# Performance work log

Measured on AMD Instinct MI355X. Metric: run time of the kernel, lower is better.

Reference implementation:

```python
import jax, jax.numpy as jnp
import numpy as np

N = 50000; E = 800000; NFEAT = 128; NHID = 64; CONCAT = 2; NCLASS = 40
D = CONCAT * NHID
BN_EPS = 1e-5


def setup_inputs() -> dict:
    key = jax.random.key(0)
    ks = jax.random.split(key, 16)
    rn = lambda k, s, sc=0.05: jax.random.normal(k, s, jnp.float32) * sc
    return {
        "x1a": rn(ks[0], (N, NFEAT), 1.0),
        "x1b": rn(ks[1], (N, NFEAT), 1.0),
        "x2a": rn(ks[2], (N, NFEAT), 1.0),
        "x2b": rn(ks[3], (N, NFEAT), 1.0),
        "edge_index1": jax.random.randint(ks[4], (2, E), 0, N),
        "edge_index2": jax.random.randint(ks[5], (2, E), 0, N),
        "Wi": rn(ks[6], (CONCAT, NFEAT, NHID)),
        "bi": jnp.zeros((CONCAT, NHID), jnp.float32),
        "gi": jnp.ones((CONCAT, NHID), jnp.float32),
        "bei": jnp.zeros((CONCAT, NHID), jnp.float32),
        "Wm": rn(ks[7], (2, D, D)),
        "bm": jnp.zeros((2, D), jnp.float32),
        "gm": jnp.ones((2, D), jnp.float32),
        "bem": jnp.zeros((2, D), jnp.float32),
        "Wf": rn(ks[8], (D, NCLASS)),
        "bf": jnp.zeros((NCLASS,), jnp.float32),
        "fc1w1_W": rn(ks[9], (D,)),
        "fc1w1_b": jnp.zeros((1,), jnp.float32),
        "fc1w2_W": rn(ks[10], (D,)),
        "fc1w2_b": jnp.zeros((1,), jnp.float32),
        "aws_w1_W": rn(ks[11], (2, D)),
        "aws_w1_b": jnp.zeros((2,), jnp.float32),
        "aws_w2_W": rn(ks[12], (2, D)),
        "aws_w2_b": jnp.zeros((2,), jnp.float32),
        "fcw1_W": rn(ks[13], (NCLASS,)),
        "fcw1_b": jnp.zeros((1,), jnp.float32),
        "fcw2_W": rn(ks[14], (NCLASS,)),
        "fcw2_b": jnp.zeros((1,), jnp.float32),
    }


def _gcn_norm(edge_index, n):
    # GCN symmetric normalization with self-loops (cached=True behaviour)
    loop = jnp.arange(n)
    src = jnp.concatenate([edge_index[0], loop])
    dst = jnp.concatenate([edge_index[1], loop])
    deg = jax.ops.segment_sum(jnp.ones_like(dst, jnp.float32), dst, n)
    dinv = jnp.where(deg > 0, deg ** -0.5, 0.0)
    return src, dst, dinv[src] * dinv[dst]


def _gcn(x, W, b, g):
    # GCNConv: dense projection then sparse scatter-based aggregation
    src, dst, norm = g
    h = x @ W
    agg = jax.ops.segment_sum(h[src] * norm[:, None], dst, x.shape[0])
    return agg + b


def _bn(x, gamma, beta):
    m = x.mean(0)
    v = jnp.mean((x - m) ** 2, axis=0)
    return (x - m) * jax.lax.rsqrt(v + BN_EPS) * gamma + beta


def _gate(x1, x2, w1, b1, w2, b2):
    # sigmoid gates L1-normalized; only the last node's row is used (w[-1,:])
    s1 = jax.nn.sigmoid(jnp.dot(x1[-1], w1) + b1)
    s2 = jax.nn.sigmoid(jnp.dot(x2[-1], w2) + b2)
    t = s1 + s2
    return s1 / t, s2 / t


def _forward(x1a, x1b, x2a, x2b, g1, g2, Wi, bi, gi, bei, Wm, bm, gm, bem,
             Wf, bf, fc1w1_W, fc1w1_b, fc1w2_W, fc1w2_b,
             aws_w1_W, aws_w1_b, aws_w2_W, aws_w2_b,
             fcw1_W, fcw1_b, fcw2_W, fcw2_b):
    xs1, xs2 = (x1a, x1b), (x2a, x2b)
    h1 = jnp.concatenate([jax.nn.relu(_bn(_gcn(xs1[i], Wi[i], bi[i], g1), gi[i], bei[i]))
                          for i in range(CONCAT)], axis=-1)
    h2 = jnp.concatenate([jax.nn.relu(_bn(_gcn(xs2[i], Wi[i], bi[i], g2), gi[i], bei[i]))
                          for i in range(CONCAT)], axis=-1)
    w1, w2 = _gate(h1, h2, fc1w1_W, fc1w1_b[0], fc1w2_W, fc1w2_b[0])
    x = w1 * h1 + w2 * h2
    for i in range(Wm.shape[0]):  # middle layers (n_layers - 2)
        a = jax.nn.relu(_bn(_gcn(x, Wm[i], bm[i], g1), gm[i], bem[i]))
        b = jax.nn.relu(_bn(_gcn(x, Wm[i], bm[i], g2), gm[i], bem[i]))
        w1, w2 = _gate(a, b, aws_w1_W[i], aws_w1_b[i], aws_w2_W[i], aws_w2_b[i])
        x = w1 * a + w2 * b
    p1 = _gcn(x, Wf, bf, g1)
    p2 = _gcn(x, Wf, bf, g2)
    w1, w2 = _gate(p1, p2, fcw1_W, fcw1_b[0], fcw2_W, fcw2_b[0])
    return (w1 * p1 + w2 * p2, p1, p2)


def reference(x1a, x1b, x2a, x2b, edge_index1, edge_index2, Wi, bi, gi, bei,
              Wm, bm, gm, bem, Wf, bf, fc1w1_W, fc1w1_b, fc1w2_W, fc1w2_b,
              aws_w1_W, aws_w1_b, aws_w2_W, aws_w2_b,
              fcw1_W, fcw1_b, fcw2_W, fcw2_b):
    g1 = _gcn_norm(edge_index1, N)
    g2 = _gcn_norm(edge_index2, N)
    return _forward(x1a, x1b, x2a, x2b, g1, g2, Wi, bi, gi, bei, Wm, bm, gm, bem,
                    Wf, bf, fc1w1_W, fc1w1_b, fc1w2_W, fc1w2_b,
                    aws_w1_W, aws_w1_b, aws_w2_W, aws_w2_b,
                    fcw1_W, fcw1_b, fcw2_W, fcw2_b)
```

## Files before the change

kernel.cpp:

```cpp
#include <hip/hip_runtime.h>
#include <hip/hip_fp16.h>


#define DFEAT 128

typedef __attribute__((ext_vector_type(8))) short bf16x8;
typedef __attribute__((ext_vector_type(4))) float f32x4;

__device__ __forceinline__ unsigned short f2bf(float f) {
    unsigned u = __float_as_uint(f);
    u += 0x7fffu + ((u >> 16) & 1u);
    return (unsigned short)(u >> 16);
}
__device__ __forceinline__ float bf2f(unsigned short u) {
    return __uint_as_float((unsigned)u << 16);
}
__device__ __forceinline__ float4 bf4tof4(ushort4 u) {
    return make_float4(__uint_as_float((unsigned)u.x << 16),
                       __uint_as_float((unsigned)u.y << 16),
                       __uint_as_float((unsigned)u.z << 16),
                       __uint_as_float((unsigned)u.w << 16));
}
__device__ __forceinline__ unsigned f2h16(float f) {
    return (unsigned)__half_as_ushort(__float2half(f));
}
__device__ __forceinline__ float h16f(unsigned u) {
    return __half2float(__ushort_as_half((unsigned short)u));
}

constexpr int RANGES = 8;
constexpr int SLICES = 32;
constexpr int MAXRSZ = 6400;

__global__ __launch_bounds__(256) void histRS_kernel(
    const int* __restrict__ dst1, const int* __restrict__ dst2,
    int* __restrict__ base, int n, int E, int rsz) {
    int range = blockIdx.x & (RANGES - 1);
    int q = blockIdx.x >> 3;
    int slice = q & (SLICES - 1);
    int graph = q >> 5;
    const int* dst = graph ? dst2 : dst1;
    int r0 = range * rsz;
    int rn = min(rsz, n - r0);
    if (rn <= 0) return;
    __shared__ int hist[MAXRSZ];
    int t = threadIdx.x;
    for (int i = t; i < rn; i += 256) hist[i] = 0;
    __syncthreads();
    int es = (E + SLICES - 1) / SLICES;
    int e0 = slice * es;
    int e1 = min(e0 + es, E);
    for (int i = e0 + t; i < e1; i += 256) {
        unsigned d = (unsigned)(dst[i] - r0);
        if (d < (unsigned)rn) atomicAdd(&hist[d], 1);
    }
    __syncthreads();
    int* bp = base + (size_t)(graph * SLICES + slice) * n + r0;
    for (int i = t; i < rn; i += 256) bp[i] = hist[i];
}

__global__ __launch_bounds__(256) void slicescan_kernel(
    int* __restrict__ base, int* __restrict__ cnt1, int* __restrict__ cnt2, int n) {
    int node = blockIdx.x * 256 + threadIdx.x;
    int g = blockIdx.y;
    if (node >= n) return;
    int* p = base + (size_t)g * SLICES * n + node;
    int run = 0;
#pragma unroll
    for (int s = 0; s < SLICES; ++s) {
        int v = p[(size_t)s * n];
        p[(size_t)s * n] = run;
        run += v;
    }
    (g ? cnt2 : cnt1)[node] = run;
}

__global__ __launch_bounds__(256) void fillRS_kernel(
    const int* __restrict__ src1, const int* __restrict__ dst1,
    const int* __restrict__ src2, const int* __restrict__ dst2,
    const int* __restrict__ base,
    const int* __restrict__ rp1, const int* __restrict__ rp2,
    const float* __restrict__ dv1, const float* __restrict__ dv2,
    int* __restrict__ cs1, int* __restrict__ cs2, int n, int E, int rsz) {
    int range = blockIdx.x & (RANGES - 1);
    int q = blockIdx.x >> 3;
    int slice = q & (SLICES - 1);
    int graph = q >> 5;
    const int *src, *dst, *rp;
    const float* dv;
    int* cs;
    if (graph == 0) { src = src1; dst = dst1; rp = rp1; dv = dv1; cs = cs1; }
    else            { src = src2; dst = dst2; rp = rp2; dv = dv2; cs = cs2; }
    int r0 = range * rsz;
    int rn = min(rsz, n - r0);
    if (rn <= 0) return;
    __shared__ int off[MAXRSZ];
    int t = threadIdx.x;
    const int* bp = base + (size_t)(graph * SLICES + slice) * n + r0;
    for (int i = t; i < rn; i += 256) off[i] = bp[i] + rp[r0 + i];
    __syncthreads();
    int es = (E + SLICES - 1) / SLICES;
    int e0 = slice * es;
    int e1 = min(e0 + es, E);
    for (int i = e0 + t; i < e1; i += 256) {
        int d = dst[i];
        unsigned dr = (unsigned)(d - r0);
        if (dr < (unsigned)rn) {
            int s = src[i];
            float w = dv[d] * dv[s];
            int pos = atomicAdd(&off[dr], 1);
            cs[pos] = (int)((f2h16(w) << 16) | (unsigned)s);
        }
    }
}

__global__ __launch_bounds__(256) void blocksum_kernel(const int* __restrict__ c1,
                                                       const int* __restrict__ c2,
                                                       int* __restrict__ bs, int n, int nb) {
    const int* c = blockIdx.y ? c2 : c1;
    int* out = bs + (size_t)blockIdx.y * nb;
    int t = threadIdx.x;
    int base = blockIdx.x * 2048 + t * 8;
    int s = 0;
#pragma unroll
    for (int i = 0; i < 8; ++i) {
        int idx = base + i;
        if (idx < n) s += c[idx];
    }
    __shared__ int red[256];
    red[t] = s;
    __syncthreads();
    for (int o = 128; o > 0; o >>= 1) {
        if (t < o) red[t] += red[t + o];
        __syncthreads();
    }
    if (t == 0) out[blockIdx.x] = red[0];
}

__global__ void scansums_kernel(int* __restrict__ bs, int nb, int* __restrict__ rp1,
                                int* __restrict__ rp2, int n, int E, float* __restrict__ stats) {
    int t = threadIdx.x;
    if (t < 2) {
        int* b = bs + (size_t)t * nb;
        int run = 0;
        for (int i = 0; i < nb; ++i) {
            int v = b[i];
            b[i] = run;
            run += v;
        }
        (t ? rp2 : rp1)[n] = E;
    }
    for (int i = t; i < 512; i += 64) stats[i] = 0.f;
}

__global__ __launch_bounds__(256) void writerp_kernel(const int* __restrict__ c1,
                                                      const int* __restrict__ c2,
                                                      const int* __restrict__ bs,
                                                      int* __restrict__ rp1, int* __restrict__ rp2,
                                                      float* __restrict__ dv1,
                                                      float* __restrict__ dv2, int n, int nb) {
    const int* c = blockIdx.y ? c2 : c1;
    int* rp = blockIdx.y ? rp2 : rp1;
    float* dv = blockIdx.y ? dv2 : dv1;
    int boff = bs[(size_t)blockIdx.y * nb + blockIdx.x];
    int t = threadIdx.x;
    int base = blockIdx.x * 2048 + t * 8;
    int v[8];
    int s = 0;
#pragma unroll
    for (int i = 0; i < 8; ++i) {
        int idx = base + i;
        v[i] = (idx < n) ? c[idx] : 0;
        s += v[i];
    }
    __shared__ int red[256];
    red[t] = s;
    __syncthreads();
    for (int o = 1; o < 256; o <<= 1) {
        int x = (t >= o) ? red[t - o] : 0;
        __syncthreads();
        red[t] += x;
        __syncthreads();
    }
    int run = boff + red[t] - s;
#pragma unroll
    for (int i = 0; i < 8; ++i) {
        int idx = base + i;
        if (idx < n) {
            rp[idx] = run;
            dv[idx] = rsqrtf((float)(v[i] + 1));
            run += v[i];
        }
    }
}

template <int FV, typename OutT>
__global__ __launch_bounds__(256) void dualagg_kernel(
    const unsigned short* __restrict__ h1, const unsigned short* __restrict__ h2,
    const int* __restrict__ rp1, const int* __restrict__ cs1, const float* __restrict__ dv1,
    const int* __restrict__ rp2, const int* __restrict__ cs2, const float* __restrict__ dv2,
    const float* __restrict__ bias, OutT* __restrict__ o1, OutT* __restrict__ o2, int n) {
    constexpr int COLS = FV * 4;
    const unsigned short* h;
    const int *rp, *cs;
    const float* dv;
    OutT* out;
    if (blockIdx.y == 0) { h = h1; rp = rp1; cs = cs1; dv = dv1; out = o1; }
    else                 { h = h2; rp = rp2; cs = cs2; dv = dv2; out = o2; }
    int wid = blockIdx.x * 4 + (threadIdx.x >> 6);
    if (wid >= n) return;
    int lane = threadIdx.x & 63;
    int half = lane >> 5;
    int l = lane & 31;
    bool act = (l < FV);
    float4 acc = make_float4(0.f, 0.f, 0.f, 0.f);
    int e0 = rp[wid], e1 = rp[wid + 1];
    int e = e0 + half;
    for (; e + 6 < e1; e += 8) {
        int va = cs[e], vb = cs[e + 2], vc = cs[e + 4], vd = cs[e + 6];
        float wa = h16f((unsigned)va >> 16); int sa = va & 0xFFFF;
        float wb = h16f((unsigned)vb >> 16); int sb = vb & 0xFFFF;
        float wc = h16f((unsigned)vc >> 16); int sc = vc & 0xFFFF;
        float wd = h16f((unsigned)vd >> 16); int sd = vd & 0xFFFF;
        if (act) {
            float4 ha = bf4tof4(((const ushort4*)(h + (size_t)sa * COLS))[l]);
            float4 hb = bf4tof4(((const ushort4*)(h + (size_t)sb * COLS))[l]);
            float4 hc = bf4tof4(((const ushort4*)(h + (size_t)sc * COLS))[l]);
            float4 hd = bf4tof4(((const ushort4*)(h + (size_t)sd * COLS))[l]);
            acc.x = fmaf(wa, ha.x, acc.x); acc.y = fmaf(wa, ha.y, acc.y);
            acc.z = fmaf(wa, ha.z, acc.z); acc.w = fmaf(wa, ha.w, acc.w);
            acc.x = fmaf(wb, hb.x, acc.x); acc.y = fmaf(wb, hb.y, acc.y);
            acc.z = fmaf(wb, hb.z, acc.z); acc.w = fmaf(wb, hb.w, acc.w);
            acc.x = fmaf(wc, hc.x, acc.x); acc.y = fmaf(wc, hc.y, acc.y);
            acc.z = fmaf(wc, hc.z, acc.z); acc.w = fmaf(wc, hc.w, acc.w);
            acc.x = fmaf(wd, hd.x, acc.x); acc.y = fmaf(wd, hd.y, acc.y);
            acc.z = fmaf(wd, hd.z, acc.z); acc.w = fmaf(wd, hd.w, acc.w);
        }
    }
    for (; e < e1; e += 2) {
        int va = cs[e];
        float wa = h16f((unsigned)va >> 16); int sa = va & 0xFFFF;
        if (act) {
            float4 ha = bf4tof4(((const ushort4*)(h + (size_t)sa * COLS))[l]);
            acc.x = fmaf(wa, ha.x, acc.x); acc.y = fmaf(wa, ha.y, acc.y);
            acc.z = fmaf(wa, ha.z, acc.z); acc.w = fmaf(wa, ha.w, acc.w);
        }
    }
    acc.x += __shfl_xor(acc.x, 32);
    acc.y += __shfl_xor(acc.y, 32);
    acc.z += __shfl_xor(acc.z, 32);
    acc.w += __shfl_xor(acc.w, 32);
    if (half == 0 && act) {
        float dn = dv[wid];
        float w = dn * dn;
        float4 hv = bf4tof4(((const ushort4*)(h + (size_t)wid * COLS))[l]);
        acc.x = fmaf(w, hv.x, acc.x); acc.y = fmaf(w, hv.y, acc.y);
        acc.z = fmaf(w, hv.z, acc.z); acc.w = fmaf(w, hv.w, acc.w);
        float4 b = ((const float4*)bias)[l];
        acc.x += b.x; acc.y += b.y; acc.z += b.z; acc.w += b.w;
        if constexpr (sizeof(OutT) == 4) {
            ((float4*)((float*)out + (size_t)wid * COLS))[l] = acc;
        } else {
            ushort4 o;
            o.x = f2bf(acc.x); o.y = f2bf(acc.y); o.z = f2bf(acc.z); o.w = f2bf(acc.w);
            ((ushort4*)((unsigned short*)out + (size_t)wid * COLS))[l] = o;
        }
    }
}

__global__ __launch_bounds__(256) void gemm_l1_kernel(
    const float* __restrict__ x1a, const float* __restrict__ x1b, const float* __restrict__ x2a,
    const float* __restrict__ x2b, const float* __restrict__ Wi, unsigned short* __restrict__ H1,
    unsigned short* __restrict__ H2, int nrows) {
    constexpr int CG = 16;
    const float* X = (blockIdx.y == 0) ? x1a : (blockIdx.y == 1) ? x1b
                     : (blockIdx.y == 2) ? x2a : x2b;
    const float* W = Wi + (blockIdx.y & 1) * 128 * 64;
    unsigned short* Y = (blockIdx.y < 2) ? H1 : H2;
    int ocol = (int)(blockIdx.y & 1) * 64;
    __shared__ float Ws[32][64];
    __shared__ float Xs[64][32];
    int tid = threadIdx.x;
    int row0 = blockIdx.x * 64;
    int cg = tid % CG;
    int rg = tid / CG;
    float4 acc[4];
#pragma unroll
    for (int i = 0; i < 4; ++i) acc[i] = make_float4(0.f, 0.f, 0.f, 0.f);
    for (int kc = 0; kc < 4; ++kc) {
        for (int i = tid; i < 32 * CG; i += 256) {
            int r = i / CG, c = i % CG;
            *(float4*)&Ws[r][c * 4] = *(const float4*)(W + (size_t)(kc * 32 + r) * 64 + c * 4);
        }
        for (int i = tid; i < 64 * 8; i += 256) {
            int r = i / 8, c = i % 8;
            int gr = row0 + r;
            float4 v = make_float4(0.f, 0.f, 0.f, 0.f);
            if (gr < nrows) v = *(const float4*)(X + (size_t)gr * DFEAT + kc * 32 + c * 4);
            *(float4*)&Xs[r][c * 4] = v;
        }
        __syncthreads();
#pragma unroll
        for (int k = 0; k < 32; ++k) {
            float4 w = *(float4*)&Ws[k][cg * 4];
#pragma unroll
            for (int i = 0; i < 4; ++i) {
                float a = Xs[rg * 4 + i][k];
                acc[i].x = fmaf(a, w.x, acc[i].x);
                acc[i].y = fmaf(a, w.y, acc[i].y);
                acc[i].z = fmaf(a, w.z, acc[i].z);
                acc[i].w = fmaf(a, w.w, acc[i].w);
            }
        }
        __syncthreads();
    }
#pragma unroll
    for (int i = 0; i < 4; ++i) {
        int r = row0 + rg * 4 + i;
        if (r < nrows) {
            ushort4 o;
            o.x = f2bf(acc[i].x); o.y = f2bf(acc[i].y);
            o.z = f2bf(acc[i].z); o.w = f2bf(acc[i].w);
            *(ushort4*)(Y + (size_t)r * DFEAT + ocol + cg * 4) = o;
        }
    }
}

__global__ __launch_bounds__(256) void prepW_kernel(const float* __restrict__ Wm,
                                                    unsigned short* __restrict__ Wt) {
    int o = blockIdx.x * 256 + threadIdx.x;
    int l = blockIdx.y;
    int kk = o & 31;
    int col = (o >> 5) & 127;
    int kc = o >> 12;
    int k = kc * 32 + kk;
    Wt[(size_t)l * 16384 + o] = f2bf(Wm[(size_t)l * 16384 + (size_t)k * 128 + col]);
}

__global__ __launch_bounds__(256) void gemm_mfma_kernel(
    const unsigned short* __restrict__ Abf, const unsigned short* __restrict__ Bbf,
    const float* __restrict__ ss, const float* __restrict__ wout,
    const unsigned short* __restrict__ Wt, unsigned short* __restrict__ Y, int nrows) {
    __shared__ short Xs[64][128];
    int tid = threadIdx.x;
    int row0 = blockIdx.x * 64;
    int wave = tid >> 6, lane = tid & 63;
    int m = lane & 15, quad = lane >> 4;
    float w1 = wout[0], w2 = wout[1];
    for (int u = tid; u < 1024; u += 256) {
        int r = u >> 4;
        int col0 = (u & 15) * 8;
        int gr = row0 + r;
        if (gr < nrows) {
#pragma unroll
            for (int hh = 0; hh < 2; ++hh) {
                int c = col0 + hh * 4;
                float4 fa = bf4tof4(*(const ushort4*)(Abf + (size_t)gr * 128 + c));
                float4 fb = bf4tof4(*(const ushort4*)(Bbf + (size_t)gr * 128 + c));
                float4 sa = *(const float4*)(ss + c);
                float4 ha = *(const float4*)(ss + 128 + c);
                float4 sb = *(const float4*)(ss + 256 + c);
                float4 hb = *(const float4*)(ss + 384 + c);
                ushort4 o;
                o.x = f2bf(w1 * fmaxf(fmaf(fa.x, sa.x, ha.x), 0.f) +
                           w2 * fmaxf(fmaf(fb.x, sb.x, hb.x), 0.f));
                o.y = f2bf(w1 * fmaxf(fmaf(fa.y, sa.y, ha.y), 0.f) +
                           w2 * fmaxf(fmaf(fb.y, sb.y, hb.y), 0.f));
                o.z = f2bf(w1 * fmaxf(fmaf(fa.z, sa.z, ha.z), 0.f) +
                           w2 * fmaxf(fmaf(fb.z, sb.z, hb.z), 0.f));
                o.w = f2bf(w1 * fmaxf(fmaf(fa.w, sa.w, ha.w), 0.f) +
                           w2 * fmaxf(fmaf(fb.w, sb.w, hb.w), 0.f));
                *(ushort4*)&Xs[r][c] = o;
            }
        } else {
            ushort4 z = {0, 0, 0, 0};
            *(ushort4*)&Xs[r][col0] = z;
            *(ushort4*)&Xs[r][col0 + 4] = z;
        }
    }
    __syncthreads();
    f32x4 acc[8];
#pragma unroll
    for (int i = 0; i < 8; ++i) acc[i] = (f32x4){0.f, 0.f, 0.f, 0.f};
#pragma unroll
    for (int kc = 0; kc < 4; ++kc) {
        bf16x8 a = *(const bf16x8*)&Xs[wave * 16 + m][kc * 32 + quad * 8];
#pragma unroll
        for (int ct = 0; ct < 8; ++ct) {
            const short* bp = (const short*)(Wt + ((size_t)(kc * 128 + ct * 16 + m) * 32) + quad * 8);
            bf16x8 b = *(const bf16x8*)bp;
            acc[ct] = __builtin_amdgcn_mfma_f32_16x16x32_bf16(a, b, acc[ct], 0, 0, 0);
        }
    }
#pragma unroll
    for (int ct = 0; ct < 8; ++ct) {
#pragma unroll
        for (int i = 0; i < 4; ++i) {
            int gr = row0 + wave * 16 + quad * 4 + i;
            if (gr < nrows) Y[(size_t)gr * 128 + ct * 16 + m] = f2bf(acc[ct][i]);
        }
    }
}

template <int CG, int RPT>
__global__ __launch_bounds__(256) void gemm_fused_kernel(
    const unsigned short* __restrict__ Abf, const unsigned short* __restrict__ Bbf,
    const float* __restrict__ ss, const float* __restrict__ wout, const float* __restrict__ W,
    unsigned short* __restrict__ Y, int nrows, int fout, int ostride) {
    __shared__ float Ws[32][CG * 4];
    __shared__ float Xs[64][32];
    int tid = threadIdx.x;
    int row0 = blockIdx.x * 64;
    int cg = tid % CG;
    int rg = tid / CG;
    float w1 = wout[0], w2 = wout[1];
    float4 acc[RPT];
#pragma unroll
    for (int i = 0; i < RPT; ++i) acc[i] = make_float4(0.f, 0.f, 0.f, 0.f);
    for (int kc = 0; kc < 4; ++kc) {
        for (int i = tid; i < 32 * CG; i += 256) {
            int r = i / CG, c = i % CG;
            float4 w;
            if ((c * 4 + 3) < fout) {
                w = *(const float4*)(W + (size_t)(kc * 32 + r) * fout + c * 4);
            } else {
                float t0 = (c * 4 + 0) < fout ? W[(size_t)(kc * 32 + r) * fout + c * 4 + 0] : 0.f;
                float t1 = (c * 4 + 1) < fout ? W[(size_t)(kc * 32 + r) * fout + c * 4 + 1] : 0.f;
                float t2 = (c * 4 + 2) < fout ? W[(size_t)(kc * 32 + r) * fout + c * 4 + 2] : 0.f;
                float t3 = (c * 4 + 3) < fout ? W[(size_t)(kc * 32 + r) * fout + c * 4 + 3] : 0.f;
                w = make_float4(t0, t1, t2, t3);
            }
            *(float4*)&Ws[r][c * 4] = w;
        }
        for (int i = tid; i < 64 * 8; i += 256) {
            int r = i / 8, c = i % 8;
            int gr = row0 + r;
            int col0 = kc * 32 + c * 4;
            float4 v = make_float4(0.f, 0.f, 0.f, 0.f);
            if (gr < nrows) {
                float4 a = bf4tof4(*(const ushort4*)(Abf + (size_t)gr * DFEAT + col0));
                float4 b = bf4tof4(*(const ushort4*)(Bbf + (size_t)gr * DFEAT + col0));
                float4 scA = *(const float4*)(ss + col0);
                float4 shA = *(const float4*)(ss + DFEAT + col0);
                float4 scB = *(const float4*)(ss + 2 * DFEAT + col0);
                float4 shB = *(const float4*)(ss + 3 * DFEAT + col0);
                v.x = w1 * fmaxf(fmaf(a.x, scA.x, shA.x), 0.f) +
                      w2 * fmaxf(fmaf(b.x, scB.x, shB.x), 0.f);
                v.y = w1 * fmaxf(fmaf(a.y, scA.y, shA.y), 0.f) +
                      w2 * fmaxf(fmaf(b.y, scB.y, shB.y), 0.f);
                v.z = w1 * fmaxf(fmaf(a.z, scA.z, shA.z), 0.f) +
                      w2 * fmaxf(fmaf(b.z, scB.z, shB.z), 0.f);
                v.w = w1 * fmaxf(fmaf(a.w, scA.w, shA.w), 0.f) +
                      w2 * fmaxf(fmaf(b.w, scB.w, shB.w), 0.f);
            }
            *(float4*)&Xs[r][c * 4] = v;
        }
        __syncthreads();
#pragma unroll
        for (int k = 0; k < 32; ++k) {
            float4 w = *(float4*)&Ws[k][cg * 4];
#pragma unroll
            for (int i = 0; i < RPT; ++i) {
                float a = Xs[rg * RPT + i][k];
                acc[i].x = fmaf(a, w.x, acc[i].x);
                acc[i].y = fmaf(a, w.y, acc[i].y);
                acc[i].z = fmaf(a, w.z, acc[i].z);
                acc[i].w = fmaf(a, w.w, acc[i].w);
            }
        }
        __syncthreads();
    }
    if (cg * 4 < fout) {
#pragma unroll
        for (int i = 0; i < RPT; ++i) {
            int r = row0 + rg * RPT + i;
            if (r < nrows) {
                ushort4 o;
                o.x = f2bf(acc[i].x); o.y = f2bf(acc[i].y);
                o.z = f2bf(acc[i].z); o.w = f2bf(acc[i].w);
                *(ushort4*)(Y + (size_t)r * ostride + cg * 4) = o;
            }
        }
    }
}

__global__ __launch_bounds__(256) void stats2_kernel(const unsigned short* __restrict__ A,
                                                     const unsigned short* __restrict__ B,
                                                     float* __restrict__ stats, int nrows) {
    __shared__ float red1[256];
    __shared__ float red2[256];
    int t = threadIdx.x;
    int col = t & 127;
    int rg = t >> 7;
    const unsigned short* src = (blockIdx.y == 0) ? A : B;
    float* st = stats + (size_t)blockIdx.y * 256;
    int r0 = blockIdx.x * 128 + rg * 64;
    int r1 = min(r0 + 64, nrows);
    float s = 0.f, s2 = 0.f;
    for (int r = r0; r < r1; ++r) {
        float v = bf2f(src[(size_t)r * DFEAT + col]);
        s += v;
        s2 = fmaf(v, v, s2);
    }
    red1[t] = s;
    red2[t] = s2;
    __syncthreads();
    if (t < 128) {
        atomicAdd(&st[col], red1[t] + red1[t + 128]);
        atomicAdd(&st[DFEAT + col], red2[t] + red2[t + 128]);
    }
}

__global__ __launch_bounds__(128) void gate_prep_kernel(
    float* __restrict__ statsA, float* __restrict__ statsB,
    const unsigned short* __restrict__ preA, const unsigned short* __restrict__ preB,
    const float* __restrict__ gamma, const float* __restrict__ beta,
    const float* __restrict__ gwA, const float* __restrict__ gbA,
    const float* __restrict__ gwB, const float* __restrict__ gbB,
    float* __restrict__ ss, float* __restrict__ wout, int nrows) {
    __shared__ float red[128];
    __shared__ float dotA_s;
    int t = threadIdx.x;
    float invN = 1.f / (float)nrows;
    float meanA = statsA[t] * invN;
    float varA = statsA[DFEAT + t] * invN - meanA * meanA;
    float scA = gamma[t] * rsqrtf(varA + 1e-5f);
    float shA = beta[t] - meanA * scA;
    ss[t] = scA;
    ss[DFEAT + t] = shA;
    float meanB = statsB[t] * invN;
    float varB = statsB[DFEAT + t] * invN - meanB * meanB;
    float scB = gamma[t] * rsqrtf(varB + 1e-5f);
    float shB = beta[t] - meanB * scB;
    ss[2 * DFEAT + t] = scB;
    ss[3 * DFEAT + t] = shB;
    statsA[t] = 0.f;
    statsA[DFEAT + t] = 0.f;
    statsB[t] = 0.f;
    statsB[DFEAT + t] = 0.f;
    float av = fmaxf(fmaf(bf2f(preA[(size_t)(nrows - 1) * DFEAT + t]), scA, shA), 0.f);
    red[t] = av * gwA[t];
    __syncthreads();
    for (int s = 64; s > 0; s >>= 1) {
        if (t < s) red[t] += red[t + s];
        __syncthreads();
    }
    if (t == 0) dotA_s = red[0];
    __syncthreads();
    float bv = fmaxf(fmaf(bf2f(preB[(size_t)(nrows - 1) * DFEAT + t]), scB, shB), 0.f);
    red[t] = bv * gwB[t];
    __syncthreads();
    for (int s = 64; s > 0; s >>= 1) {
        if (t < s) red[t] += red[t + s];
        __syncthreads();
    }
    if (t == 0) {
        float s1 = 1.f / (1.f + expf(-(dotA_s + gbA[0])));
        float s2 = 1.f / (1.f + expf(-(red[0] + gbB[0])));
        float tt = s1 + s2;
        wout[0] = s1 / tt;
        wout[1] = s2 / tt;
    }
}

__global__ __launch_bounds__(64) void gate_final_kernel(
    const float* __restrict__ p1, const float* __restrict__ p2,
    const float* __restrict__ w1v, const float* __restrict__ b1,
    const float* __restrict__ w2v, const float* __restrict__ b2,
    float* __restrict__ wout, int nrows, int nclass) {
    __shared__ float red[64];
    __shared__ float dot1_s;
    int t = threadIdx.x;
    float v = (t < nclass) ? p1[(size_t)(nrows - 1) * nclass + t] * w1v[t] : 0.f;
    red[t] = v;
    __syncthreads();
    for (int s = 32; s > 0; s >>= 1) {
        if (t < s) red[t] += red[t + s];
        __syncthreads();
    }
    if (t == 0) dot1_s = red[0];
    __syncthreads();
    v = (t < nclass) ? p2[(size_t)(nrows - 1) * nclass + t] * w2v[t] : 0.f;
    red[t] = v;
    __syncthreads();
    for (int s = 32; s > 0; s >>= 1) {
        if (t < s) red[t] += red[t + s];
        __syncthreads();
    }
    if (t == 0) {
        float s1 = 1.f / (1.f + expf(-(dot1_s + b1[0])));
        float s2 = 1.f / (1.f + expf(-(red[0] + b2[0])));
        float tt = s1 + s2;
        wout[0] = s1 / tt;
        wout[1] = s2 / tt;
    }
}

__global__ __launch_bounds__(256) void mix_kernel(const float* __restrict__ p1,
                                                  const float* __restrict__ p2,
                                                  const float* __restrict__ wout,
                                                  float* __restrict__ o, int n4) {
    int idx = blockIdx.x * blockDim.x + threadIdx.x;
    if (idx >= n4) return;
    float w1 = wout[0], w2 = wout[1];
    float4 a = *(const float4*)(p1 + (size_t)idx * 4);
    float4 b = *(const float4*)(p2 + (size_t)idx * 4);
    float4 r = make_float4(w1 * a.x + w2 * b.x, w1 * a.y + w2 * b.y, w1 * a.z + w2 * b.z,
                           w1 * a.w + w2 * b.w);
    *(float4*)(o + (size_t)idx * 4) = r;
}

extern "C" void kernel_launch(void* const* d_in, const int* in_sizes, int n_in, void* d_out,
                              int out_size, void* d_ws, size_t ws_size, hipStream_t stream) {
    (void)n_in; (void)out_size; (void)ws_size;
    const int N = in_sizes[0] / DFEAT;
    const int E = in_sizes[4] / 2;
    const int NC = in_sizes[15];

    const float* x1a = (const float*)d_in[0];
    const float* x1b = (const float*)d_in[1];
    const float* x2a = (const float*)d_in[2];
    const float* x2b = (const float*)d_in[3];
    const int* ei1 = (const int*)d_in[4];
    const int* ei2 = (const int*)d_in[5];
    const float* Wi = (const float*)d_in[6];
    const float* bi = (const float*)d_in[7];
    const float* gi = (const float*)d_in[8];
    const float* bei = (const float*)d_in[9];
    const float* Wm = (const float*)d_in[10];
    const float* bm = (const float*)d_in[11];
    const float* gm = (const float*)d_in[12];
    const float* bem = (const float*)d_in[13];
    const float* Wf = (const float*)d_in[14];
    const float* bf = (const float*)d_in[15];
    const float* fc1w1_W = (const float*)d_in[16];
    const float* fc1w1_b = (const float*)d_in[17];
    const float* fc1w2_W = (const float*)d_in[18];
    const float* fc1w2_b = (const float*)d_in[19];
    const float* aws_w1_W = (const float*)d_in[20];
    const float* aws_w1_b = (const float*)d_in[21];
    const float* aws_w2_W = (const float*)d_in[22];
    const float* aws_w2_b = (const float*)d_in[23];
    const float* fcw1_W = (const float*)d_in[24];
    const float* fcw1_b = (const float*)d_in[25];
    const float* fcw2_W = (const float*)d_in[26];
    const float* fcw2_b = (const float*)d_in[27];

    char* ws = (char*)d_ws;
    size_t off = 0;
    auto alloc = [&](size_t bytes) -> char* {
        char* p = ws + off;
        off += (bytes + 255) & ~(size_t)255;
        return p;
    };
    unsigned short* A = (unsigned short*)alloc((size_t)N * DFEAT * 2);
    unsigned short* B = (unsigned short*)alloc((size_t)N * DFEAT * 2);
    unsigned short* H1 = (unsigned short*)alloc((size_t)N * DFEAT * 2);
    unsigned short* H2 = (unsigned short*)alloc((size_t)N * DFEAT * 2);
    int* rp1 = (int*)alloc((size_t)(N + 1) * 4);
    int* rp2 = (int*)alloc((size_t)(N + 1) * 4);
    int* cnt1 = (int*)alloc((size_t)N * 4);
    int* cnt2 = (int*)alloc((size_t)N * 4);
    float* dv1 = (float*)alloc((size_t)N * 4);
    float* dv2 = (float*)alloc((size_t)N * 4);
    int* cs1 = (int*)alloc((size_t)E * 4);
    int* cs2 = (int*)alloc((size_t)E * 4);
    int* base = (int*)alloc((size_t)2 * SLICES * N * 4);
    unsigned short* Wt = (unsigned short*)alloc((size_t)2 * 16384 * 2);
    float* stats = (float*)alloc(2048);
    float* statsA = stats;
    float* statsB = stats + 256;
    float* ssbuf = (float*)alloc(2048);
    float* wout = (float*)alloc(256);
    int nb = (N + 2047) / 2048;
    int* bsums = (int*)alloc((size_t)2 * nb * 4);

    const int* src1 = ei1;
    const int* dst1 = ei1 + E;
    const int* src2 = ei2;
    const int* dst2 = ei2 + E;

    int rsz = (N + RANGES - 1) / RANGES;
    int gemmbl = (N + 63) / 64;
    dim3 rsgrid(RANGES * SLICES * 2);
    dim3 ssgrid((N + 255) / 256, 2);
    dim3 agggrid((N + 3) / 4, 2);
    dim3 statgrid((N + 127) / 128, 2);
    dim3 scangrid(nb, 2);
    dim3 l1grid(gemmbl, 4);
    dim3 prepgrid(64, 2);

    prepW_kernel<<<prepgrid, 256, 0, stream>>>(Wm, Wt);
    histRS_kernel<<<rsgrid, 256, 0, stream>>>(dst1, dst2, base, N, E, rsz);
    slicescan_kernel<<<ssgrid, 256, 0, stream>>>(base, cnt1, cnt2, N);
    blocksum_kernel<<<scangrid, 256, 0, stream>>>(cnt1, cnt2, bsums, N, nb);
    scansums_kernel<<<1, 64, 0, stream>>>(bsums, nb, rp1, rp2, N, E, stats);
    writerp_kernel<<<scangrid, 256, 0, stream>>>(cnt1, cnt2, bsums, rp1, rp2, dv1, dv2, N, nb);
    fillRS_kernel<<<rsgrid, 256, 0, stream>>>(src1, dst1, src2, dst2, base, rp1, rp2,
                                              dv1, dv2, cs1, cs2, N, E, rsz);

    gemm_l1_kernel<<<l1grid, 256, 0, stream>>>(x1a, x1b, x2a, x2b, Wi, H1, H2, N);
    dualagg_kernel<32, unsigned short><<<agggrid, 256, 0, stream>>>(
        H1, H2, rp1, cs1, dv1, rp2, cs2, dv2, bi, A, B, N);
    stats2_kernel<<<statgrid, 256, 0, stream>>>(A, B, stats, N);
    gate_prep_kernel<<<1, 128, 0, stream>>>(statsA, statsB, A, B, gi, bei, fc1w1_W, fc1w1_b,
                                            fc1w2_W, fc1w2_b, ssbuf, wout, N);

    gemm_mfma_kernel<<<gemmbl, 256, 0, stream>>>(A, B, ssbuf, wout, Wt, H1, N);
    dualagg_kernel<32, unsigned short><<<agggrid, 256, 0, stream>>>(
        H1, H1, rp1, cs1, dv1, rp2, cs2, dv2, bm, A, B, N);
    stats2_kernel<<<statgrid, 256, 0, stream>>>(A, B, stats, N);
    gate_prep_kernel<<<1, 128, 0, stream>>>(statsA, statsB, A, B, gm, bem, aws_w1_W, aws_w1_b,
                                            aws_w2_W, aws_w2_b, ssbuf, wout, N);

    gemm_mfma_kernel<<<gemmbl, 256, 0, stream>>>(A, B, ssbuf, wout, Wt + 16384, H1, N);
    dualagg_kernel<32, unsigned short><<<agggrid, 256, 0, stream>>>(
        H1, H1, rp1, cs1, dv1, rp2, cs2, dv2, bm + 128, A, B, N);
    stats2_kernel<<<statgrid, 256, 0, stream>>>(A, B, stats, N);
    gate_prep_kernel<<<1, 128, 0, stream>>>(statsA, statsB, A, B, gm + 128, bem + 128,
                                            aws_w1_W + 128, aws_w1_b + 1, aws_w2_W + 128,
                                            aws_w2_b + 1, ssbuf, wout, N);

    float* out0 = (float*)d_out;
    float* p1 = out0 + (size_t)N * NC;
    float* p2 = out0 + (size_t)2 * N * NC;
    gemm_fused_kernel<16, 4><<<gemmbl, 256, 0, stream>>>(A, B, ssbuf, wout, Wf, H2, N, NC, NC);
    dualagg_kernel<10, float><<<agggrid, 256, 0, stream>>>(H2, H2, rp1, cs1, dv1, rp2, cs2, dv2,
                                                           bf, p1, p2, N);
    gate_final_kernel<<<1, 64, 0, stream>>>(p1, p2, fcw1_W, fcw1_b, fcw2_W, fcw2_b, wout, N, NC);
    mix_kernel<<<(N * NC / 4 + 255) / 256, 256, 0, stream>>>(p1, p2, wout, out0, N * NC / 4);
}
```

Baseline: 757.6 us.

## Replace sliced range-scan CSR build with two-pass radix partition of edges

The CSR construction previously had every block scan all edges and keep only those whose destination fell in its node range, so each edge was read once per range. Now a first pass buckets packed (dst,src) pairs into 8192-node ranges in a staging buffer through global atomic counters. Per-range histogram, scan and fill kernels then read only their own bucket. This cuts redundant edge reads, at the cost of an extra staging write/read, a memset, nondeterministic edge order within each node, and reliance on node ids fitting in 16 bits and bucket sizes fitting a fixed capacity.

```diff
diff --git a/kernel.cpp b/kernel.cpp
--- a/kernel.cpp
+++ b/kernel.cpp
@@ -28,89 +28,131 @@
     return __half2float(__ushort_as_half((unsigned short)u));
 }
 
-constexpr int RANGES = 8;
-constexpr int SLICES = 32;
-constexpr int MAXRSZ = 6400;
-
-__global__ __launch_bounds__(256) void histRS_kernel(
-    const int* __restrict__ dst1, const int* __restrict__ dst2,
-    int* __restrict__ base, int n, int E, int rsz) {
-    int range = blockIdx.x & (RANGES - 1);
-    int q = blockIdx.x >> 3;
-    int slice = q & (SLICES - 1);
-    int graph = q >> 5;
-    const int* dst = graph ? dst2 : dst1;
-    int r0 = range * rsz;
-    int rn = min(rsz, n - r0);
-    if (rn <= 0) return;
-    __shared__ int hist[MAXRSZ];
-    int t = threadIdx.x;
-    for (int i = t; i < rn; i += 256) hist[i] = 0;
-    __syncthreads();
-    int es = (E + SLICES - 1) / SLICES;
-    int e0 = slice * es;
-    int e1 = min(e0 + es, E);
+constexpr int RSH = 13;
+constexpr int RSZ = 8192;
+constexpr int NRMAX = 8;
+constexpr int EPA = 2048;
+constexpr int SUBS = 16;
+constexpr int SCAP = 160000;
+
+__global__ __launch_bounds__(256) void partA_kernel(
+    const int* __restrict__ src1, const int* __restrict__ dst1,
+    const int* __restrict__ src2, const int* __restrict__ dst2,
+    int* __restrict__ stg, int* __restrict__ gcount, int E, int nr) {
+    int g = blockIdx.y;
+    const int* src = g ? src2 : src1;
+    const int* dst = g ? dst2 : dst1;
+    __shared__ int buf[EPA];
+    __shared__ int buf2[EPA];
+    __shared__ int cnt8[NRMAX + 1], pre8[NRMAX + 1], base8[NRMAX];
+    int t = threadIdx.x;
+    if (t < NRMAX) cnt8[t] = 0;
+    __syncthreads();
+    int e0 = blockIdx.x * EPA;
+    int e1 = min(e0 + EPA, E);
+    int ec = e1 - e0;
     for (int i = e0 + t; i < e1; i += 256) {
-        unsigned d = (unsigned)(dst[i] - r0);
-        if (d < (unsigned)rn) atomicAdd(&hist[d], 1);
-    }
-    __syncthreads();
-    int* bp = base + (size_t)(graph * SLICES + slice) * n + r0;
-    for (int i = t; i < rn; i += 256) bp[i] = hist[i];
-}
-
-__global__ __launch_bounds__(256) void slicescan_kernel(
-    int* __restrict__ base, int* __restrict__ cnt1, int* __restrict__ cnt2, int n) {
+        int d = dst[i];
+        int s = src[i];
+        buf[i - e0] = (d << 16) | s;
+        atomicAdd(&cnt8[d >> RSH], 1);
+    }
+    __syncthreads();
+    if (t == 0) {
+        int run = 0;
+        for (int r = 0; r < nr; ++r) { pre8[r] = run; run += cnt8[r]; }
+        pre8[nr] = run;
+    }
+    __syncthreads();
+    if (t < nr) {
+        base8[t] = atomicAdd(&gcount[g * NRMAX + t], cnt8[t]);
+        cnt8[t] = 0;
+    }
+    __syncthreads();
+    for (int j = t; j < ec; j += 256) {
+        int v = buf[j];
+        int d = (unsigned)v >> 16;
+        int r = d >> RSH;
+        int p = pre8[r] + atomicAdd(&cnt8[r], 1);
+        buf2[p] = ((d & (RSZ - 1)) << 16) | (v & 0xFFFF);
+    }
+    __syncthreads();
+    for (int j = t; j < ec; j += 256) {
+        int r = 0;
+        while (j >= pre8[r + 1]) ++r;
+        int gpos = base8[r] + (j - pre8[r]);
+        if (gpos < SCAP) stg[((size_t)g * NRMAX + r) * SCAP + gpos] = buf2[j];
+    }
+}
+
+__global__ __launch_bounds__(256) void histB_kernel(
+    const int* __restrict__ stg, const int* __restrict__ gcount,
+    int* __restrict__ baseB, int nr) {
+    int g = blockIdx.y;
+    int r = blockIdx.x / SUBS;
+    int sub = blockIdx.x % SUBS;
+    __shared__ int hist[RSZ];
+    int t = threadIdx.x;
+    for (int i = t; i < RSZ; i += 256) hist[i] = 0;
+    __syncthreads();
+    int len = min(gcount[g * NRMAX + r], SCAP);
+    int seg = (len + SUBS - 1) / SUBS;
+    int e0 = sub * seg, e1 = min(e0 + seg, len);
+    const int* sp = stg + ((size_t)g * NRMAX + r) * SCAP;
+    for (int i = e0 + t; i < e1; i += 256) atomicAdd(&hist[(unsigned)sp[i] >> 16], 1);
+    __syncthreads();
+    int* bp = baseB + (((size_t)(g * NRMAX + r) * SUBS + sub) << RSH);
+    for (int i = t; i < RSZ; i += 256) bp[i] = hist[i];
+}
+
+__global__ __launch_bounds__(256) void scanB_kernel(
+    int* __restrict__ baseB, int* __restrict__ cnt1, int* __restrict__ cnt2, int n) {
     int node = blockIdx.x * 256 + threadIdx.x;
     int g = blockIdx.y;
     if (node >= n) return;
-    int* p = base + (size_t)g * SLICES * n + node;
+    int r = node >> RSH, dloc = node & (RSZ - 1);
+    int* p = baseB + (((size_t)(g * NRMAX + r) * SUBS) << RSH) + dloc;
     int run = 0;
 #pragma unroll
-    for (int s = 0; s < SLICES; ++s) {
-        int v = p[(size_t)s * n];
-        p[(size_t)s * n] = run;
+    for (int s = 0; s < SUBS; ++s) {
+        int v = p[(size_t)s << RSH];
+        p[(size_t)s << RSH] = run;
         run += v;
     }
     (g ? cnt2 : cnt1)[node] = run;
 }
 
-__global__ __launch_bounds__(256) void fillRS_kernel(
-    const int* __restrict__ src1, const int* __restrict__ dst1,
-    const int* __restrict__ src2, const int* __restrict__ dst2,
-    const int* __restrict__ base,
+__global__ __launch_bounds__(256) void fillC_kernel(
+    const int* __restrict__ stg, const int* __restrict__ gcount,
+    const int* __restrict__ baseB,
     const int* __restrict__ rp1, const int* __restrict__ rp2,
     const float* __restrict__ dv1, const float* __restrict__ dv2,
-    int* __restrict__ cs1, int* __restrict__ cs2, int n, int E, int rsz) {
-    int range = blockIdx.x & (RANGES - 1);
-    int q = blockIdx.x >> 3;
-    int slice = q & (SLICES - 1);
-    int graph = q >> 5;
-    const int *src, *dst, *rp;
-    const float* dv;
-    int* cs;
-    if (graph == 0) { src = src1; dst = dst1; rp = rp1; dv = dv1; cs = cs1; }
-    else            { src = src2; dst = dst2; rp = rp2; dv = dv2; cs = cs2; }
-    int r0 = range * rsz;
-    int rn = min(rsz, n - r0);
+    int* __restrict__ cs1, int* __restrict__ cs2, int n, int nr) {
+    int g = blockIdx.y;
+    int r = blockIdx.x / SUBS;
+    int sub = blockIdx.x % SUBS;
+    const int* rp = g ? rp2 : rp1;
+    const float* dv = g ? dv2 : dv1;
+    int* cs = g ? cs2 : cs1;
+    __shared__ int off[RSZ];
+    int t = threadIdx.x;
+    int r0 = r << RSH;
+    int rn = min(RSZ, n - r0);
     if (rn <= 0) return;
-    __shared__ int off[MAXRSZ];
-    int t = threadIdx.x;
-    const int* bp = base + (size_t)(graph * SLICES + slice) * n + r0;
+    const int* bp = baseB + (((size_t)(g * NRMAX + r) * SUBS + sub) << RSH);
     for (int i = t; i < rn; i += 256) off[i] = bp[i] + rp[r0 + i];
     __syncthreads();
-    int es = (E + SLICES - 1) / SLICES;
-    int e0 = slice * es;
-    int e1 = min(e0 + es, E);
+    int len = min(gcount[g * NRMAX + r], SCAP);
+    int seg = (len + SUBS - 1) / SUBS;
+    int e0 = sub * seg, e1 = min(e0 + seg, len);
+    const int* sp = stg + ((size_t)g * NRMAX + r) * SCAP;
     for (int i = e0 + t; i < e1; i += 256) {
-        int d = dst[i];
-        unsigned dr = (unsigned)(d - r0);
-        if (dr < (unsigned)rn) {
-            int s = src[i];
-            float w = dv[d] * dv[s];
-            int pos = atomicAdd(&off[dr], 1);
-            cs[pos] = (int)((f2h16(w) << 16) | (unsigned)s);
-        }
+        int v = sp[i];
+        int dloc = (unsigned)v >> 16;
+        int s = v & 0xFFFF;
+        float w = dv[r0 + dloc] * dv[s];
+        int pos = atomicAdd(&off[dloc], 1);
+        cs[pos] = (int)((f2h16(w) << 16) | (unsigned)s);
     }
 }
 
@@ -665,7 +707,9 @@
     float* dv2 = (float*)alloc((size_t)N * 4);
     int* cs1 = (int*)alloc((size_t)E * 4);
     int* cs2 = (int*)alloc((size_t)E * 4);
-    int* base = (int*)alloc((size_t)2 * SLICES * N * 4);
+    int* stg = (int*)alloc((size_t)2 * NRMAX * SCAP * 4);
+    int* baseB = (int*)alloc(((size_t)2 * NRMAX * SUBS << RSH) * 4);
+    int* gcount = (int*)alloc(2 * NRMAX * 4);
     unsigned short* Wt = (unsigned short*)alloc((size_t)2 * 16384 * 2);
     float* stats = (float*)alloc(2048);
     float* statsA = stats;
@@ -680,9 +724,10 @@
     const int* src2 = ei2;
     const int* dst2 = ei2 + E;
 
-    int rsz = (N + RANGES - 1) / RANGES;
+    int nr = (N + RSZ - 1) >> RSH;
     int gemmbl = (N + 63) / 64;
-    dim3 rsgrid(RANGES * SLICES * 2);
+    dim3 pagrid((E + EPA - 1) / EPA, 2);
+    dim3 rsgrid(nr * SUBS, 2);
     dim3 ssgrid((N + 255) / 256, 2);
     dim3 agggrid((N + 3) / 4, 2);
     dim3 statgrid((N + 127) / 128, 2);
@@ -690,14 +735,16 @@
     dim3 l1grid(gemmbl, 4);
     dim3 prepgrid(64, 2);
 
+    hipMemsetAsync(gcount, 0, 2 * NRMAX * 4, stream);
     prepW_kernel<<<prepgrid, 256, 0, stream>>>(Wm, Wt);
-    histRS_kernel<<<rsgrid, 256, 0, stream>>>(dst1, dst2, base, N, E, rsz);
-    slicescan_kernel<<<ssgrid, 256, 0, stream>>>(base, cnt1, cnt2, N);
+    partA_kernel<<<pagrid, 256, 0, stream>>>(src1, dst1, src2, dst2, stg, gcount, E, nr);
+    histB_kernel<<<rsgrid, 256, 0, stream>>>(stg, gcount, baseB, nr);
+    scanB_kernel<<<ssgrid, 256, 0, stream>>>(baseB, cnt1, cnt2, N);
     blocksum_kernel<<<scangrid, 256, 0, stream>>>(cnt1, cnt2, bsums, N, nb);
     scansums_kernel<<<1, 64, 0, stream>>>(bsums, nb, rp1, rp2, N, E, stats);
     writerp_kernel<<<scangrid, 256, 0, stream>>>(cnt1, cnt2, bsums, rp1, rp2, dv1, dv2, N, nb);
-    fillRS_kernel<<<rsgrid, 256, 0, stream>>>(src1, dst1, src2, dst2, base, rp1, rp2,
-                                              dv1, dv2, cs1, cs2, N, E, rsz);
+    fillC_kernel<<<rsgrid, 256, 0, stream>>>(stg, gcount, baseB, rp1, rp2, dv1, dv2,
+                                             cs1, cs2, N, nr);
 
     gemm_l1_kernel<<<l1grid, 256, 0, stream>>>(x1a, x1b, x2a, x2b, Wi, H1, H2, N);
     dualagg_kernel<32, unsigned short><<<agggrid, 256, 0, stream>>>(
```

Measured after the change: 688.6 us. 1.1x faster.
